# Performance work log

Hardware: AMD Instinct MI355X
Metric: run time of the kernel (lower is better)

## Reference

```python
import jax, jax.numpy as jnp
import numpy as np
from jax import lax

LOKAL_GRUP = 7
TOP_K = 2
EPS = 1e-8
CACHE_BONUS = 0.1


def setup_inputs() -> dict:
    key = jax.random.key(0)
    ks = jax.random.split(key, 6)
    B, S, D, E, H = 2, 2048, 1024, 8, 4096
    return {
        "x": jax.random.normal(ks[0], (B, S, D), jnp.float32),
        "uzman_embeddings": jax.random.normal(ks[1], (E, D), jnp.float32) * 0.01,
        "W1": jax.random.normal(ks[2], (E, D, H), jnp.float32) * 0.02,
        "b1": jax.random.normal(ks[3], (E, H), jnp.float32) * 0.02,
        "W2": jax.random.normal(ks[4], (E, H, D), jnp.float32) * 0.02,
        "b2": jax.random.normal(ks[5], (E, D), jnp.float32) * 0.02,
        "onbellek_durumu": jnp.ones((E,), jnp.float32),
    }


def _route(tokens, uzman_embeddings, onbellek_durumu):
    # tokens: [N, D], uzman_embeddings: [E, D]
    # local group selection: top LOKAL_GRUP experts by raw dot product
    sim = tokens @ uzman_embeddings.T                      # [N, E]
    _, local_idx = lax.top_k(sim, LOKAL_GRUP)              # [N, LG]
    # cosine scores within local group
    t_norm = tokens / (jnp.linalg.norm(tokens, axis=-1, keepdims=True) + EPS)
    e_norm = uzman_embeddings / (jnp.linalg.norm(uzman_embeddings, axis=-1, keepdims=True) + EPS)
    local_embs = e_norm[local_idx]                         # [N, LG, D]
    scores = jnp.einsum("nld,nd->nl", local_embs, t_norm)
    scores = scores + CACHE_BONUS * onbellek_durumu[local_idx]
    top_scores, top_local = lax.top_k(scores, TOP_K)       # [N, K]
    global_idx = jnp.take_along_axis(local_idx, top_local, axis=1)  # [N, K]
    weights = jax.nn.softmax(top_scores, axis=-1)          # [N, K]
    # original computes routing in detached numpy -> no grad through gate
    return global_idx, lax.stop_gradient(weights)


def reference(x, uzman_embeddings, W1, b1, W2, b2, onbellek_durumu):
    B, S, D = x.shape
    tokens = x.reshape(-1, D)                              # [N, D]
    global_idx, weights = _route(tokens, uzman_embeddings, onbellek_durumu)
    # run every expert on every token (dense), then gather the top-k outputs
    h = jnp.einsum("nd,edh->enh", tokens, W1) + b1[:, None, :]   # [E, N, H]
    h = jax.nn.gelu(h, approximate=False)                         # torch nn.GELU exact
    out_all = jnp.einsum("enh,ehd->end", h, W2) + b2[:, None, :]  # [E, N, D]
    N = tokens.shape[0]
    out_sel = out_all[global_idx, jnp.arange(N)[:, None]]         # [N, K, D]
    out = jnp.sum(weights[..., None] * out_sel, axis=1)           # [N, D]
    return out.reshape(B, S, D)
```

## Files before the change

kernel.cpp:

```cpp
#include <hip/hip_runtime.h>
#include <hip/hip_bf16.h>

#define NTOK 4096
#define DDIM 1024
#define HDIM 4096
#define NEXP 8
#define NPAIR (NTOK * 2)
#define BMT 256
#define MAXT 40

typedef __attribute__((ext_vector_type(8))) short bf16x8;
typedef __attribute__((ext_vector_type(4))) float f32x4;

struct Misc {
  float enorm[NEXP];
  int cnt[NEXP];
  int cursor[NEXP];
  int nt;
  int pad;
  int te[MAXT];
  int tp0[MAXT];
  int tp1[MAXT];
  int gidx[NTOK * 2];
  float twt[NTOK * 2];
  int ppos[NTOK * 2];
  int rows[NPAIR];
  float pwt[NPAIR];
};

#define OFF_W2T 0ull
#define OFF_H 0x4000000ull
#define OFF_XG 0x8000000ull
#define OFF_W1T 0x9000000ull
#define OFF_OUTP 0x8000000ull
#define OFF_MISC 0xD000000ull

__device__ __forceinline__ unsigned short f2bf(float f) {
  unsigned int u = __float_as_uint(f);
  u += 0x7fffu + ((u >> 16) & 1u);
  return (unsigned short)(u >> 16);
}

__global__ __launch_bounds__(512) void enorm_k(const float* __restrict__ emb, Misc* mi) {
  int w = threadIdx.x >> 6, l = threadIdx.x & 63;
  const float* r = emb + (size_t)w * DDIM;
  float s = 0.f;
  for (int i = l; i < DDIM; i += 64) {
    float v = r[i];
    s += v * v;
  }
  #pragma unroll
  for (int o = 32; o; o >>= 1) s += __shfl_xor(s, o);
  if (l == 0) mi->enorm[w] = sqrtf(s);
}

__global__ __launch_bounds__(64) void route_k(const float* __restrict__ x,
                                              const float* __restrict__ emb,
                                              const float* __restrict__ cache, Misc* mi) {
  int n = blockIdx.x, l = threadIdx.x;
  const float* xr = x + (size_t)n * DDIM;
  float s[NEXP];
  #pragma unroll
  for (int e = 0; e < NEXP; e++) s[e] = 0.f;
  float nr = 0.f;
  for (int i = l; i < DDIM; i += 64) {
    float xv = xr[i];
    nr += xv * xv;
    #pragma unroll
    for (int e = 0; e < NEXP; e++) s[e] += xv * emb[e * DDIM + i];
  }
  #pragma unroll
  for (int o = 32; o; o >>= 1) {
    nr += __shfl_xor(nr, o);
    #pragma unroll
    for (int e = 0; e < NEXP; e++) s[e] += __shfl_xor(s[e], o);
  }
  if (l == 0) {
    float tn = sqrtf(nr) + 1e-8f;
    int exc = 0;
    float mn = s[0];
    for (int e = 1; e < NEXP; e++)
      if (s[e] <= mn) {
        mn = s[e];
        exc = e;
      }
    float sc[NEXP];
    for (int e = 0; e < NEXP; e++)
      sc[e] = s[e] / (tn * (mi->enorm[e] + 1e-8f)) + 0.1f * cache[e];
    int g0 = -1, g1 = -1;
    for (int e = 0; e < NEXP; e++) {
      if (e == exc) continue;
      if (g0 < 0 || sc[e] > sc[g0] || (sc[e] == sc[g0] && s[e] > s[g0])) g0 = e;
    }
    for (int e = 0; e < NEXP; e++) {
      if (e == exc || e == g0) continue;
      if (g1 < 0 || sc[e] > sc[g1] || (sc[e] == sc[g1] && s[e] > s[g1])) g1 = e;
    }
    float e1 = expf(sc[g1] - sc[g0]);
    float w0 = 1.f / (1.f + e1);
    float w1 = e1 * w0;
    mi->gidx[2 * n] = g0;
    mi->gidx[2 * n + 1] = g1;
    mi->twt[2 * n] = w0;
    mi->twt[2 * n + 1] = w1;
    atomicAdd(mi->cnt + g0, 1);
    atomicAdd(mi->cnt + g1, 1);
  }
}

__global__ void scan_k(Misc* mi) {
  if (threadIdx.x != 0) return;
  int off = 0, t = 0;
  for (int e = 0; e < NEXP; e++) {
    mi->cursor[e] = off;
    int c = mi->cnt[e];
    for (int r = 0; r < c; r += BMT) {
      mi->te[t] = e;
      mi->tp0[t] = off + r;
      int hi = (r + BMT < c) ? (r + BMT) : c;
      mi->tp1[t] = off + hi;
      t++;
    }
    off += c;
  }
  mi->nt = t;
}

__global__ __launch_bounds__(256) void scatter_k(Misc* mi) {
  int n = blockIdx.x * 256 + threadIdx.x;
  if (n >= NTOK) return;
  #pragma unroll
  for (int k = 0; k < 2; k++) {
    int e = mi->gidx[2 * n + k];
    int p = atomicAdd(mi->cursor + e, 1);
    mi->rows[p] = n;
    mi->pwt[p] = mi->twt[2 * n + k];
    mi->ppos[2 * n + k] = p;
  }
}

__global__ __launch_bounds__(64) void gather_k(const float* __restrict__ x, const Misc* __restrict__ mi,
                                               unsigned short* __restrict__ xg) {
  int p = blockIdx.x, l = threadIdx.x;
  const float4* src = (const float4*)(x + (size_t)mi->rows[p] * DDIM);
  uint2* dst = (uint2*)(xg + (size_t)p * DDIM);
  #pragma unroll
  for (int j = 0; j < 4; j++) {
    float4 v = src[l + j * 64];
    uint2 o;
    o.x = (unsigned)f2bf(v.x) | ((unsigned)f2bf(v.y) << 16);
    o.y = (unsigned)f2bf(v.z) | ((unsigned)f2bf(v.w) << 16);
    dst[l + j * 64] = o;
  }
}

__global__ __launch_bounds__(256) void wconv_k(const float* __restrict__ in,
                                               unsigned short* __restrict__ out, int R, int C) {
  __shared__ float tile[64][65];
  int e = blockIdx.z;
  size_t base = (size_t)e * R * C;
  int c0 = blockIdx.x * 64, r0 = blockIdx.y * 64;
  int t = threadIdx.x;
  #pragma unroll
  for (int i = 0; i < 16; i++) {
    int idx = i * 256 + t;
    int r = idx >> 6, c = idx & 63;
    tile[r][c] = in[base + (size_t)(r0 + r) * C + (c0 + c)];
  }
  __syncthreads();
  #pragma unroll
  for (int i = 0; i < 16; i++) {
    int idx = i * 256 + t;
    int r = idx >> 6, c = idx & 63;
    out[base + (size_t)(c0 + r) * R + (r0 + c)] = f2bf(tile[c][r]);
  }
}

#define GL(src, off)                                                                        \
  __builtin_amdgcn_global_load_lds((const __attribute__((address_space(1))) void*)(src),    \
                                   (__attribute__((address_space(3))) void*)(LDS + (off)),  \
                                   16, 0, 0)

template <int MODE>
__global__ __launch_bounds__(512, 2) void gemm8_k(const unsigned short* __restrict__ A,
                                                  const unsigned short* __restrict__ B,
                                                  const float* __restrict__ bias,
                                                  unsigned short* __restrict__ hout,
                                                  float* __restrict__ outp,
                                                  const Misc* __restrict__ mi, int K, int N,
                                                  int nk) {
  __shared__ char LDS[131072];
  int nwg = gridDim.x * gridDim.y * gridDim.z;
  int lin = (blockIdx.z * gridDim.y + blockIdx.y) * gridDim.x + blockIdx.x;
  int q = nwg >> 3, r = nwg & 7, xc = lin & 7;
  int wk = (xc < r ? xc * (q + 1) : r * (q + 1) + (xc - r) * q) + (lin >> 3);
  int nb = wk % gridDim.x;
  int rest = wk / gridDim.x;
  int tb = rest % gridDim.y;
  int ks = rest / gridDim.y;
  if (tb >= mi->nt) return;
  int e = mi->te[tb], p0 = mi->tp0[tb], p1 = mi->tp1[tb];
  int n0 = nb * 256;
  int k0 = ks * nk;
  int tid = threadIdx.x, w = tid >> 6, l = tid & 63;
  int wr = w >> 2, wc = w & 3;
  int srow = l >> 3;
  int scol = ((l & 7) ^ srow) << 4;
  size_t ldb = (size_t)K * 2;
  const char* Asrc[4];
  const char* Bsrc[4];
  #pragma unroll
  for (int j = 0; j < 4; j++) {
    int ar = p0 + j * 64 + w * 8 + srow;
    if (ar > NPAIR - 1) ar = NPAIR - 1;
    Asrc[j] = (const char*)A + (size_t)ar * ldb + scol;
    int br = n0 + j * 64 + w * 8 + srow;
    Bsrc[j] = (const char*)B + (size_t)e * N * ldb + (size_t)br * ldb + scol;
  }
  f32x4 acc[8][4];
  f32x4 zero = {0.f, 0.f, 0.f, 0.f};
  #pragma unroll
  for (int m = 0; m < 8; m++)
    #pragma unroll
    for (int n = 0; n < 4; n++) acc[m][n] = zero;
  int q4 = l >> 4, s3 = l & 7;
  int colk0 = ((q4 ^ (s3 & 3)) << 4) | ((s3 >> 2) << 6);
  int aoffB = (wr * 128 + (l & 15)) * 128 + colk0;
  int boffB = 32768 + (wc * 64 + (l & 15)) * 128 + colk0;

  long kb0 = (long)k0 * 128;
  #pragma unroll
  for (int j = 0; j < 4; j++) GL(Asrc[j] + kb0, j * 8192 + w * 1024);
  #pragma unroll
  for (int j = 0; j < 4; j++) GL(Bsrc[j] + kb0, 32768 + j * 8192 + w * 1024);
  if (nk > 1) {
    GL(Asrc[0] + kb0 + 128, 65536 + w * 1024);
    GL(Asrc[1] + kb0 + 128, 65536 + 8192 + w * 1024);
  }

  bf16x8 af[4][2], bf[4][2];
  for (int t = 0; t < nk; ++t) {
    int cb = (t & 1) << 16, nbuf = ((t + 1) & 1) << 16;
    long kb1 = (long)(k0 + t + 1) * 128;
    long kb2 = kb1 + 128;
    int ao = cb + aoffB, bo = cb + boffB;
    bool ld1 = (t + 1 < nk), ld2 = (t + 2 < nk);
    if (ld1)
      asm volatile("s_waitcnt vmcnt(2)" ::: "memory");
    else
      asm volatile("s_waitcnt vmcnt(0)" ::: "memory");
    __builtin_amdgcn_s_barrier();
    asm volatile("" ::: "memory");
    if (ld1) {
      GL(Asrc[2] + kb1, nbuf + 2 * 8192 + w * 1024);
      GL(Asrc[3] + kb1, nbuf + 3 * 8192 + w * 1024);
    }
    #pragma unroll
    for (int m = 0; m < 4; m++)
      #pragma unroll
      for (int kk = 0; kk < 2; kk++)
        af[m][kk] = *(const bf16x8*)(LDS + ((ao + m * 2048) ^ (kk << 6)));
    #pragma unroll
    for (int n = 0; n < 2; n++)
      #pragma unroll
      for (int kk = 0; kk < 2; kk++)
        bf[n][kk] = *(const bf16x8*)(LDS + ((bo + n * 2048) ^ (kk << 6)));
    asm volatile("s_waitcnt lgkmcnt(0)" ::: "memory");
    __builtin_amdgcn_sched_barrier(0);
    __builtin_amdgcn_s_setprio(1);
    #pragma unroll
    for (int m = 0; m < 4; m++)
      #pragma unroll
      for (int n = 0; n < 2; n++)
        #pragma unroll
        for (int kk = 0; kk < 2; kk++)
          acc[m][n] = __builtin_amdgcn_mfma_f32_16x16x32_bf16(af[m][kk], bf[n][kk], acc[m][n], 0, 0, 0);
    __builtin_amdgcn_s_setprio(0);
    __builtin_amdgcn_s_barrier();
    asm volatile("" ::: "memory");
    if (ld1) {
      GL(Bsrc[0] + kb1, nbuf + 32768 + w * 1024);
      GL(Bsrc[1] + kb1, nbuf + 32768 + 8192 + w * 1024);
    }
    #pragma unroll
    for (int n = 0; n < 2; n++)
      #pragma unroll
      for (int kk = 0; kk < 2; kk++)
        bf[2 + n][kk] = *(const bf16x8*)(LDS + ((bo + (2 + n) * 2048) ^ (kk << 6)));
    asm volatile("s_waitcnt lgkmcnt(0)" ::: "memory");
    __builtin_amdgcn_sched_barrier(0);
    __builtin_amdgcn_s_setprio(1);
    #pragma unroll
    for (int m = 0; m < 4; m++)
      #pragma unroll
      for (int n = 0; n < 2; n++)
        #pragma unroll
        for (int kk = 0; kk < 2; kk++)
          acc[m][2 + n] = __builtin_amdgcn_mfma_f32_16x16x32_bf16(af[m][kk], bf[2 + n][kk], acc[m][2 + n], 0, 0, 0);
    __builtin_amdgcn_s_setprio(0);
    __builtin_amdgcn_s_barrier();
    asm volatile("" ::: "memory");
    if (ld1) {
      GL(Bsrc[2] + kb1, nbuf + 32768 + 2 * 8192 + w * 1024);
      GL(Bsrc[3] + kb1, nbuf + 32768 + 3 * 8192 + w * 1024);
    }
    #pragma unroll
    for (int m = 0; m < 4; m++)
      #pragma unroll
      for (int kk = 0; kk < 2; kk++)
        af[m][kk] = *(const bf16x8*)(LDS + ((ao + 8192 + m * 2048) ^ (kk << 6)));
    asm volatile("s_waitcnt lgkmcnt(0)" ::: "memory");
    __builtin_amdgcn_sched_barrier(0);
    __builtin_amdgcn_s_setprio(1);
    #pragma unroll
    for (int m = 0; m < 4; m++)
      #pragma unroll
      for (int n = 0; n < 2; n++)
        #pragma unroll
        for (int kk = 0; kk < 2; kk++)
          acc[4 + m][2 + n] = __builtin_amdgcn_mfma_f32_16x16x32_bf16(af[m][kk], bf[2 + n][kk], acc[4 + m][2 + n], 0, 0, 0);
    __builtin_amdgcn_s_setprio(0);
    __builtin_amdgcn_s_barrier();
    asm volatile("" ::: "memory");
    if (ld2) {
      GL(Asrc[0] + kb2, cb + w * 1024);
      GL(Asrc[1] + kb2, cb + 8192 + w * 1024);
    }
    __builtin_amdgcn_s_setprio(1);
    #pragma unroll
    for (int m = 0; m < 4; m++)
      #pragma unroll
      for (int n = 0; n < 2; n++)
        #pragma unroll
        for (int kk = 0; kk < 2; kk++)
          acc[4 + m][n] = __builtin_amdgcn_mfma_f32_16x16x32_bf16(af[m][kk], bf[n][kk], acc[4 + m][n], 0, 0, 0);
    __builtin_amdgcn_s_setprio(0);
    __builtin_amdgcn_s_barrier();
    asm volatile("" ::: "memory");
  }
  int cbase = n0 + wc * 64 + (l & 15);
  if (MODE == 0) {
    float bv[4];
    #pragma unroll
    for (int n = 0; n < 4; n++) bv[n] = bias[e * N + cbase + n * 16];
    #pragma unroll
    for (int m = 0; m < 8; m++) {
      #pragma unroll
      for (int jj = 0; jj < 4; jj++) {
        int pr = p0 + wr * 128 + m * 16 + q4 * 4 + jj;
        if (pr >= p1) continue;
        #pragma unroll
        for (int n = 0; n < 4; n++) {
          float v = acc[m][n][jj] + bv[n];
          float g = 0.5f * v * (1.f + erff(v * 0.70710678118654752f));
          hout[(size_t)pr * N + cbase + n * 16] = f2bf(g);
        }
      }
    }
  } else {
    float* op = outp + (size_t)ks * NPAIR * DDIM;
    #pragma unroll
    for (int m = 0; m < 8; m++) {
      #pragma unroll
      for (int jj = 0; jj < 4; jj++) {
        int pr = p0 + wr * 128 + m * 16 + q4 * 4 + jj;
        if (pr >= p1) continue;
        #pragma unroll
        for (int n = 0; n < 4; n++) op[(size_t)pr * N + cbase + n * 16] = acc[m][n][jj];
      }
    }
  }
}

__global__ __launch_bounds__(256) void combine_k(const float* __restrict__ op,
                                                 const float* __restrict__ b2,
                                                 const Misc* __restrict__ mi,
                                                 float* __restrict__ out) {
  int tok = blockIdx.x, i = threadIdx.x;
  int pa = mi->ppos[2 * tok], pb = mi->ppos[2 * tok + 1];
  float w0 = mi->twt[2 * tok], w1 = mi->twt[2 * tok + 1];
  int e0 = mi->gidx[2 * tok], e1 = mi->gidx[2 * tok + 1];
  const float4* o0 = (const float4*)op;
  const float4* o1 = (const float4*)(op + (size_t)NPAIR * DDIM);
  float4 r0a = o0[(size_t)pa * 256 + i], r1a = o1[(size_t)pa * 256 + i];
  float4 r0b = o0[(size_t)pb * 256 + i], r1b = o1[(size_t)pb * 256 + i];
  float4 va = ((const float4*)(b2 + (size_t)e0 * DDIM))[i];
  float4 vb = ((const float4*)(b2 + (size_t)e1 * DDIM))[i];
  float4 res;
  res.x = w0 * (r0a.x + r1a.x + va.x) + w1 * (r0b.x + r1b.x + vb.x);
  res.y = w0 * (r0a.y + r1a.y + va.y) + w1 * (r0b.y + r1b.y + vb.y);
  res.z = w0 * (r0a.z + r1a.z + va.z) + w1 * (r0b.z + r1b.z + vb.z);
  res.w = w0 * (r0a.w + r1a.w + va.w) + w1 * (r0b.w + r1b.w + vb.w);
  ((float4*)out)[(size_t)tok * 256 + i] = res;
}

extern "C" void kernel_launch(void* const* d_in, const int* in_sizes, int n_in, void* d_out,
                              int out_size, void* d_ws, size_t ws_size, hipStream_t stream) {
  const float* x = (const float*)d_in[0];
  const float* emb = (const float*)d_in[1];
  const float* W1 = (const float*)d_in[2];
  const float* b1 = (const float*)d_in[3];
  const float* W2 = (const float*)d_in[4];
  const float* b2 = (const float*)d_in[5];
  const float* cache = (const float*)d_in[6];
  float* out = (float*)d_out;
  char* ws = (char*)d_ws;
  unsigned short* W1T = (unsigned short*)(ws + OFF_W1T);
  unsigned short* W2T = (unsigned short*)(ws + OFF_W2T);
  unsigned short* hb = (unsigned short*)(ws + OFF_H);
  unsigned short* xg = (unsigned short*)(ws + OFF_XG);
  float* outp = (float*)(ws + OFF_OUTP);
  Misc* mi = (Misc*)(ws + OFF_MISC);

  hipMemsetAsync(mi, 0, sizeof(Misc), stream);

  enorm_k<<<1, 512, 0, stream>>>(emb, mi);
  route_k<<<NTOK, 64, 0, stream>>>(x, emb, cache, mi);
  scan_k<<<1, 1, 0, stream>>>(mi);
  scatter_k<<<NTOK / 256, 256, 0, stream>>>(mi);
  gather_k<<<NPAIR, 64, 0, stream>>>(x, mi, xg);
  wconv_k<<<dim3(HDIM / 64, DDIM / 64, NEXP), 256, 0, stream>>>(W1, W1T, DDIM, HDIM);
  wconv_k<<<dim3(DDIM / 64, HDIM / 64, NEXP), 256, 0, stream>>>(W2, W2T, HDIM, DDIM);
  gemm8_k<0><<<dim3(HDIM / 256, MAXT, 1), 512, 0, stream>>>(xg, W1T, b1, hb, nullptr, mi, DDIM, HDIM, 16);
  gemm8_k<1><<<dim3(DDIM / 256, MAXT, 2), 512, 0, stream>>>(hb, W2T, nullptr, nullptr, outp, mi, HDIM, DDIM, 32);
  combine_k<<<NTOK, 256, 0, stream>>>(outp, b2, mi, out);
}
```

Baseline: 747.0 us.

## Restructure GEMM pipeline barriers, group tile scheduling, vectorize weight convert, pack small kernels

```diff
diff --git a/kernel.cpp b/kernel.cpp
--- a/kernel.cpp
+++ b/kernel.cpp
@@ -54,10 +54,10 @@
   if (l == 0) mi->enorm[w] = sqrtf(s);
 }
 
-__global__ __launch_bounds__(64) void route_k(const float* __restrict__ x,
-                                              const float* __restrict__ emb,
-                                              const float* __restrict__ cache, Misc* mi) {
-  int n = blockIdx.x, l = threadIdx.x;
+__global__ __launch_bounds__(256) void route_k(const float* __restrict__ x,
+                                               const float* __restrict__ emb,
+                                               const float* __restrict__ cache, Misc* mi) {
+  int n = blockIdx.x * 4 + (threadIdx.x >> 6), l = threadIdx.x & 63;
   const float* xr = x + (size_t)n * DDIM;
   float s[NEXP];
   #pragma unroll
@@ -109,21 +109,24 @@
 }
 
 __global__ void scan_k(Misc* mi) {
-  if (threadIdx.x != 0) return;
-  int off = 0, t = 0;
-  for (int e = 0; e < NEXP; e++) {
-    mi->cursor[e] = off;
+  int l = threadIdx.x;
+  if (l >= NEXP) return;
+  int offs = 0, toff = 0;
+  for (int e = 0; e < l; e++) {
     int c = mi->cnt[e];
-    for (int r = 0; r < c; r += BMT) {
-      mi->te[t] = e;
-      mi->tp0[t] = off + r;
-      int hi = (r + BMT < c) ? (r + BMT) : c;
-      mi->tp1[t] = off + hi;
-      t++;
-    }
-    off += c;
-  }
-  mi->nt = t;
+    offs += c;
+    toff += (c + BMT - 1) / BMT;
+  }
+  int c = mi->cnt[l];
+  mi->cursor[l] = offs;
+  int ntl = (c + BMT - 1) / BMT;
+  for (int r = 0; r < ntl; r++) {
+    mi->te[toff + r] = l;
+    mi->tp0[toff + r] = offs + r * BMT;
+    int hi = (r + 1) * BMT < c ? (r + 1) * BMT : c;
+    mi->tp1[toff + r] = offs + hi;
+  }
+  if (l == NEXP - 1) mi->nt = toff + ntl;
 }
 
 __global__ __launch_bounds__(256) void scatter_k(Misc* mi) {
@@ -139,9 +142,9 @@
   }
 }
 
-__global__ __launch_bounds__(64) void gather_k(const float* __restrict__ x, const Misc* __restrict__ mi,
-                                               unsigned short* __restrict__ xg) {
-  int p = blockIdx.x, l = threadIdx.x;
+__global__ __launch_bounds__(256) void gather_k(const float* __restrict__ x, const Misc* __restrict__ mi,
+                                                unsigned short* __restrict__ xg) {
+  int p = blockIdx.x * 4 + (threadIdx.x >> 6), l = threadIdx.x & 63;
   const float4* src = (const float4*)(x + (size_t)mi->rows[p] * DDIM);
   uint2* dst = (uint2*)(xg + (size_t)p * DDIM);
   #pragma unroll
@@ -161,18 +164,26 @@
   size_t base = (size_t)e * R * C;
   int c0 = blockIdx.x * 64, r0 = blockIdx.y * 64;
   int t = threadIdx.x;
-  #pragma unroll
-  for (int i = 0; i < 16; i++) {
-    int idx = i * 256 + t;
-    int r = idx >> 6, c = idx & 63;
-    tile[r][c] = in[base + (size_t)(r0 + r) * C + (c0 + c)];
+  int tr = t >> 4, tc = t & 15;
+  #pragma unroll
+  for (int i = 0; i < 4; i++) {
+    int row = i * 16 + tr;
+    float4 v = *(const float4*)(in + base + (size_t)(r0 + row) * C + c0 + tc * 4);
+    tile[row][tc * 4 + 0] = v.x;
+    tile[row][tc * 4 + 1] = v.y;
+    tile[row][tc * 4 + 2] = v.z;
+    tile[row][tc * 4 + 3] = v.w;
   }
   __syncthreads();
   #pragma unroll
-  for (int i = 0; i < 16; i++) {
-    int idx = i * 256 + t;
-    int r = idx >> 6, c = idx & 63;
-    out[base + (size_t)(c0 + r) * R + (r0 + c)] = f2bf(tile[c][r]);
+  for (int i = 0; i < 4; i++) {
+    int a = i * 16 + tr;
+    ushort4 o;
+    o.x = f2bf(tile[tc * 4 + 0][a]);
+    o.y = f2bf(tile[tc * 4 + 1][a]);
+    o.z = f2bf(tile[tc * 4 + 2][a]);
+    o.w = f2bf(tile[tc * 4 + 3][a]);
+    *(ushort4*)(out + base + (size_t)(c0 + a) * R + r0 + tc * 4) = o;
   }
 }
 
@@ -188,17 +199,27 @@
                                                   unsigned short* __restrict__ hout,
                                                   float* __restrict__ outp,
                                                   const Misc* __restrict__ mi, int K, int N,
-                                                  int nk) {
+                                                  int nk, int GT) {
   __shared__ char LDS[131072];
-  int nwg = gridDim.x * gridDim.y * gridDim.z;
   int lin = (blockIdx.z * gridDim.y + blockIdx.y) * gridDim.x + blockIdx.x;
-  int q = nwg >> 3, r = nwg & 7, xc = lin & 7;
-  int wk = (xc < r ? xc * (q + 1) : r * (q + 1) + (xc - r) * q) + (lin >> 3);
-  int nb = wk % gridDim.x;
-  int rest = wk / gridDim.x;
-  int tb = rest % gridDim.y;
-  int ks = rest / gridDim.y;
-  if (tb >= mi->nt) return;
+  int xc = lin & 7, rr = lin >> 3;
+  int nt = mi->nt;
+  int nbX = gridDim.x, nks = gridDim.z;
+  int total = nbX * nt * nks;
+  int chunkA = (total + 7) >> 3;
+  int p = xc * chunkA + rr;
+  if (rr >= chunkA || p >= total) return;
+  int per_ks = nbX * nt;
+  int ks = p / per_ks;
+  int p2 = p - ks * per_ks;
+  int gsize = GT * nbX;
+  int g = p2 / gsize;
+  int wv = p2 - g * gsize;
+  int gb = g * GT;
+  int gsz = min(GT, nt - gb);
+  int nb = wv / gsz;
+  int tb = gb + (wv - nb * gsz);
+
   int e = mi->te[tb], p0 = mi->tp0[tb], p1 = mi->tp1[tb];
   int n0 = nb * 256;
   int k0 = ks * nk;
@@ -236,7 +257,12 @@
   if (nk > 1) {
     GL(Asrc[0] + kb0 + 128, 65536 + w * 1024);
     GL(Asrc[1] + kb0 + 128, 65536 + 8192 + w * 1024);
-  }
+    asm volatile("s_waitcnt vmcnt(2)" ::: "memory");
+  } else {
+    asm volatile("s_waitcnt vmcnt(0)" ::: "memory");
+  }
+  __builtin_amdgcn_s_barrier();
+  asm volatile("" ::: "memory");
 
   bf16x8 af[4][2], bf[4][2];
   for (int t = 0; t < nk; ++t) {
@@ -245,26 +271,21 @@
     long kb2 = kb1 + 128;
     int ao = cb + aoffB, bo = cb + boffB;
     bool ld1 = (t + 1 < nk), ld2 = (t + 2 < nk);
-    if (ld1)
-      asm volatile("s_waitcnt vmcnt(2)" ::: "memory");
-    else
-      asm volatile("s_waitcnt vmcnt(0)" ::: "memory");
-    __builtin_amdgcn_s_barrier();
-    asm volatile("" ::: "memory");
+    #pragma unroll
+    for (int m = 0; m < 4; m++)
+      #pragma unroll
+      for (int kk = 0; kk < 2; kk++)
+        af[m][kk] = *(const bf16x8*)(LDS + ((ao + m * 2048) ^ (kk << 6)));
+    #pragma unroll
+    for (int n = 0; n < 2; n++)
+      #pragma unroll
+      for (int kk = 0; kk < 2; kk++)
+        bf[n][kk] = *(const bf16x8*)(LDS + ((bo + n * 2048) ^ (kk << 6)));
     if (ld1) {
       GL(Asrc[2] + kb1, nbuf + 2 * 8192 + w * 1024);
       GL(Asrc[3] + kb1, nbuf + 3 * 8192 + w * 1024);
     }
-    #pragma unroll
-    for (int m = 0; m < 4; m++)
-      #pragma unroll
-      for (int kk = 0; kk < 2; kk++)
-        af[m][kk] = *(const bf16x8*)(LDS + ((ao + m * 2048) ^ (kk << 6)));
-    #pragma unroll
-    for (int n = 0; n < 2; n++)
-      #pragma unroll
-      for (int kk = 0; kk < 2; kk++)
-        bf[n][kk] = *(const bf16x8*)(LDS + ((bo + n * 2048) ^ (kk << 6)));
+    __builtin_amdgcn_s_barrier();
     asm volatile("s_waitcnt lgkmcnt(0)" ::: "memory");
     __builtin_amdgcn_sched_barrier(0);
     __builtin_amdgcn_s_setprio(1);
@@ -278,15 +299,16 @@
     __builtin_amdgcn_s_setprio(0);
     __builtin_amdgcn_s_barrier();
     asm volatile("" ::: "memory");
+    #pragma unroll
+    for (int n = 0; n < 2; n++)
+      #pragma unroll
+      for (int kk = 0; kk < 2; kk++)
+        bf[2 + n][kk] = *(const bf16x8*)(LDS + ((bo + (2 + n) * 2048) ^ (kk << 6)));
     if (ld1) {
       GL(Bsrc[0] + kb1, nbuf + 32768 + w * 1024);
       GL(Bsrc[1] + kb1, nbuf + 32768 + 8192 + w * 1024);
     }
-    #pragma unroll
-    for (int n = 0; n < 2; n++)
-      #pragma unroll
-      for (int kk = 0; kk < 2; kk++)
-        bf[2 + n][kk] = *(const bf16x8*)(LDS + ((bo + (2 + n) * 2048) ^ (kk << 6)));
+    __builtin_amdgcn_s_barrier();
     asm volatile("s_waitcnt lgkmcnt(0)" ::: "memory");
     __builtin_amdgcn_sched_barrier(0);
     __builtin_amdgcn_s_setprio(1);
@@ -300,15 +322,16 @@
     __builtin_amdgcn_s_setprio(0);
     __builtin_amdgcn_s_barrier();
     asm volatile("" ::: "memory");
+    #pragma unroll
+    for (int m = 0; m < 4; m++)
+      #pragma unroll
+      for (int kk = 0; kk < 2; kk++)
+        af[m][kk] = *(const bf16x8*)(LDS + ((ao + 8192 + m * 2048) ^ (kk << 6)));
     if (ld1) {
       GL(Bsrc[2] + kb1, nbuf + 32768 + 2 * 8192 + w * 1024);
       GL(Bsrc[3] + kb1, nbuf + 32768 + 3 * 8192 + w * 1024);
     }
-    #pragma unroll
-    for (int m = 0; m < 4; m++)
-      #pragma unroll
-      for (int kk = 0; kk < 2; kk++)
-        af[m][kk] = *(const bf16x8*)(LDS + ((ao + 8192 + m * 2048) ^ (kk << 6)));
+    __builtin_amdgcn_s_barrier();
     asm volatile("s_waitcnt lgkmcnt(0)" ::: "memory");
     __builtin_amdgcn_sched_barrier(0);
     __builtin_amdgcn_s_setprio(1);
@@ -335,6 +358,10 @@
         for (int kk = 0; kk < 2; kk++)
           acc[4 + m][n] = __builtin_amdgcn_mfma_f32_16x16x32_bf16(af[m][kk], bf[n][kk], acc[4 + m][n], 0, 0, 0);
     __builtin_amdgcn_s_setprio(0);
+    if (ld2)
+      asm volatile("s_waitcnt vmcnt(2)" ::: "memory");
+    else if (ld1)
+      asm volatile("s_waitcnt vmcnt(0)" ::: "memory");
     __builtin_amdgcn_s_barrier();
     asm volatile("" ::: "memory");
   }
@@ -352,8 +379,8 @@
         #pragma unroll
         for (int n = 0; n < 4; n++) {
           float v = acc[m][n][jj] + bv[n];
-          float g = 0.5f * v * (1.f + erff(v * 0.70710678118654752f));
-          hout[(size_t)pr * N + cbase + n * 16] = f2bf(g);
+          float gl = 0.5f * v * (1.f + erff(v * 0.70710678118654752f));
+          hout[(size_t)pr * N + cbase + n * 16] = f2bf(gl);
         }
       }
     }
@@ -415,13 +442,13 @@
   hipMemsetAsync(mi, 0, sizeof(Misc), stream);
 
   enorm_k<<<1, 512, 0, stream>>>(emb, mi);
-  route_k<<<NTOK, 64, 0, stream>>>(x, emb, cache, mi);
-  scan_k<<<1, 1, 0, stream>>>(mi);
+  route_k<<<NTOK / 4, 256, 0, stream>>>(x, emb, cache, mi);
+  scan_k<<<1, 64, 0, stream>>>(mi);
   scatter_k<<<NTOK / 256, 256, 0, stream>>>(mi);
-  gather_k<<<NPAIR, 64, 0, stream>>>(x, mi, xg);
+  gather_k<<<NPAIR / 4, 256, 0, stream>>>(x, mi, xg);
   wconv_k<<<dim3(HDIM / 64, DDIM / 64, NEXP), 256, 0, stream>>>(W1, W1T, DDIM, HDIM);
   wconv_k<<<dim3(DDIM / 64, HDIM / 64, NEXP), 256, 0, stream>>>(W2, W2T, HDIM, DDIM);
-  gemm8_k<0><<<dim3(HDIM / 256, MAXT, 1), 512, 0, stream>>>(xg, W1T, b1, hb, nullptr, mi, DDIM, HDIM, 16);
-  gemm8_k<1><<<dim3(DDIM / 256, MAXT, 2), 512, 0, stream>>>(hb, W2T, nullptr, nullptr, outp, mi, HDIM, DDIM, 32);
+  gemm8_k<0><<<dim3(HDIM / 256, MAXT, 1), 512, 0, stream>>>(xg, W1T, b1, hb, nullptr, mi, DDIM, HDIM, 16, 4);
+  gemm8_k<1><<<dim3(DDIM / 256, MAXT, 2), 512, 0, stream>>>(hb, W2T, nullptr, nullptr, outp, mi, HDIM, DDIM, 32, 8);
   combine_k<<<NTOK, 256, 0, stream>>>(outp, b2, mi, out);
 }
```

Result: no change. 757.5 us (+1.4%).
